# Optimization experiments

Measured on AMD Instinct MI355X. Metric: run time of the kernel, lower is better.

The kernel has to match this reference:

```python
import jax, jax.numpy as jnp
import numpy as np

B_, L_, D_MODEL = 2, 2048, 2048
EXPAND = 2
D_IN = EXPAND * D_MODEL            # 4096 intermediate_size
HEADS = 64
HEAD_DIM = D_IN // HEADS           # 64
STATE = 128
NGROUPS = 1
K = 4                              # conv kernel
CONV_DIM = D_IN + 2 * NGROUPS * STATE   # 4352
PROJ = D_IN + CONV_DIM + HEADS          # 8512
CHUNK = 256
EPS = 1e-5


def setup_inputs() -> dict:
    key = jax.random.key(0)
    ks = jax.random.split(key, 4)
    return {
        "hidden_states": jax.random.normal(ks[0], (B_, L_, D_MODEL), jnp.float32),
        "in_proj_w": jax.random.normal(ks[1], (PROJ, D_MODEL), jnp.float32) * 0.02,
        "conv_w": jax.random.normal(ks[2], (CONV_DIM, K), jnp.float32) * 0.2,
        "conv_b": jnp.zeros((CONV_DIM,), jnp.float32),
        "dt_bias": jnp.ones((HEADS,), jnp.float32),
        "A_log": jnp.log(jnp.arange(1, HEADS + 1, dtype=jnp.float32)),
        "D": jnp.ones((HEADS,), jnp.float32),
        "norm_w": jnp.ones((D_IN,), jnp.float32),
        "out_proj_w": jax.random.normal(ks[3], (D_MODEL, D_IN), jnp.float32) * 0.02,
    }


def _segsum(x):
    # x: [..., T] -> lower-triangular segment sums [..., T, T]
    T = x.shape[-1]
    c = jnp.cumsum(x, axis=-1)
    seg = c[..., :, None] - c[..., None, :]
    return jnp.where(jnp.tril(jnp.ones((T, T), bool)), seg, -jnp.inf)


def _ssd(x, dA, Bm, Cm):
    # chunked SSD scan (exact math of the sequential selective scan)
    # x: [b,l,h,p] (already * dt), dA: [b,l,h], Bm/Cm: [b,l,g,n]
    b, l, h, p = x.shape
    n = Bm.shape[-1]
    c = l // CHUNK
    rep = h // Bm.shape[2]
    Bh = jnp.repeat(Bm, rep, axis=2).reshape(b, c, CHUNK, h, n)
    Ch = jnp.repeat(Cm, rep, axis=2).reshape(b, c, CHUNK, h, n)
    x = x.reshape(b, c, CHUNK, h, p)
    dA = dA.reshape(b, c, CHUNK, h).transpose(0, 3, 1, 2)       # [b,h,c,cl]
    dA_cum = jnp.cumsum(dA, axis=-1)
    Lmat = jnp.exp(_segsum(dA))                                  # [b,h,c,cl,cl]
    # intra-chunk (diagonal) contribution
    Y_diag = jnp.einsum('bcthn,bcshn,bhcts,bcshp->bcthp', Ch, Bh, Lmat, x)
    # per-chunk final states
    decay_states = jnp.exp(dA_cum[..., -1:] - dA_cum)            # [b,h,c,cl]
    states = jnp.einsum('bcshn,bhcs,bcshp->bchpn', Bh, decay_states, x)
    # inter-chunk recurrence
    chunk_decay = jnp.exp(_segsum(jnp.pad(dA_cum[..., -1], ((0, 0), (0, 0), (1, 0)))))  # [b,h,c+1,c+1]
    states = jnp.concatenate([jnp.zeros_like(states[:, :1]), states], axis=1)
    prev = jnp.einsum('bhzc,bchpn->bzhpn', chunk_decay, states)[:, :-1]  # state entering each chunk
    Y_off = jnp.einsum('bcthn,bchpn,bhct->bcthp', Ch, prev, jnp.exp(dA_cum))
    return (Y_diag + Y_off).reshape(b, l, h, p)


def reference(hidden_states, in_proj_w, conv_w, conv_b, dt_bias, A_log, D, norm_w, out_proj_w):
    b, l, _ = hidden_states.shape
    proj = hidden_states @ in_proj_w.T                     # [b,l,PROJ]
    gate = proj[..., :D_IN]
    xBC = proj[..., D_IN:D_IN + CONV_DIM]
    dt = proj[..., D_IN + CONV_DIM:]                       # [b,l,H]
    # causal depthwise conv1d (padding=K-1, truncated to seq_len) + silu
    xp = jnp.pad(xBC, ((0, 0), (K - 1, 0), (0, 0)))
    conv = conv_b + sum(conv_w[:, i] * xp[:, i:i + l, :] for i in range(K))
    xBC = jax.nn.silu(conv)
    x = xBC[..., :D_IN].reshape(b, l, HEADS, HEAD_DIM)
    Bm = xBC[..., D_IN:D_IN + NGROUPS * STATE].reshape(b, l, NGROUPS, STATE)
    Cm = xBC[..., D_IN + NGROUPS * STATE:].reshape(b, l, NGROUPS, STATE)
    dt = jax.nn.softplus(dt + dt_bias)                     # time_step_limit=(0,inf): no clamp
    A = -jnp.exp(A_log)                                    # [H]
    y = _ssd(x * dt[..., None], dt * A, Bm, Cm)            # [b,l,H,P]
    y = y + D[None, None, :, None] * x                     # skip term D*x
    y = y.reshape(b, l, D_IN)
    # MambaRMSNormGated: gate then rms-normalize
    hg = y * jax.nn.silu(gate)
    var = jnp.mean(hg * hg, axis=-1, keepdims=True)
    y = hg * jax.lax.rsqrt(var + EPS) * norm_w
    return y @ out_proj_w.T
```

## Files before the change

kernel.cpp:

```cpp
#include <hip/hip_runtime.h>
#include <hip/hip_bf16.h>
#include <cstdio>

#define LQ 2048
#define BB 2
#define BL 4096
#define DMODEL 2048
#define DIN 4096
#define NH 64
#define HD 64
#define NST 128
#define CONVD 4352
#define PROJD 8512
#define PROJ_PAD2 8704
#define PXW 4416
#define CHK 256
#define NCH 8

typedef __attribute__((ext_vector_type(8))) short short8;
typedef __attribute__((ext_vector_type(4))) float f32x4;

__device__ __forceinline__ unsigned short f2bu(float x) {
  __hip_bfloat16 h = __float2bfloat16(x);
  return __builtin_bit_cast(unsigned short, h);
}

__device__ __forceinline__ float b2f(unsigned short u) {
  return __bfloat162float(__builtin_bit_cast(__hip_bfloat16, u));
}

__device__ __forceinline__ f32x4 mfma16(short8 a, short8 b, f32x4 c) {
  return __builtin_amdgcn_mfma_f32_16x16x32_bf16(a, b, c, 0, 0, 0);
}

#define GLD16(gptr, lptr)                                                  \
  __builtin_amdgcn_global_load_lds(                                        \
      (const __attribute__((address_space(1))) void*)(gptr),               \
      (__attribute__((address_space(3))) void*)(lptr), 16, 0, 0)

__global__ void k_cast3(const float* __restrict__ s0, unsigned short* __restrict__ d0,
                        long n0,
                        const float* __restrict__ s1, unsigned short* __restrict__ d1,
                        long n1r, long n1t,
                        const float* __restrict__ s2, unsigned short* __restrict__ d2,
                        long n2) {
  const long ntot8 = (n0 + n1t + n2) >> 3;
  long i = (long)blockIdx.x * blockDim.x + threadIdx.x;
  const long stride = (long)gridDim.x * blockDim.x;
  for (; i < ntot8; i += stride) {
    const long e = i << 3;
    const float* src;
    unsigned short* dst;
    long rel, nreal;
    if (e < n0) { src = s0; dst = d0; rel = e; nreal = n0; }
    else if (e < n0 + n1t) { src = s1; dst = d1; rel = e - n0; nreal = n1r; }
    else { src = s2; dst = d2; rel = e - n0 - n1t; nreal = n2; }
    short8 pk;
    if (rel + 8 <= nreal) {
      const f32x4* sp = reinterpret_cast<const f32x4*>(src + rel);
      f32x4 v0 = sp[0], v1 = sp[1];
#pragma unroll
      for (int u = 0; u < 4; u++) {
        pk[u] = (short)f2bu(v0[u]);
        pk[4 + u] = (short)f2bu(v1[u]);
      }
    } else {
#pragma unroll
      for (int u = 0; u < 8; u++)
        pk[u] = (rel + u < nreal) ? (short)f2bu(src[rel + u]) : (short)0;
    }
    *reinterpret_cast<short8*>(dst + rel) = pk;
  }
}

__device__ __forceinline__ short8 rdfrag(const unsigned short (*mp)[64], int rowbase,
                                         int lane, int kh) {
  const int row = rowbase + (lane & 15);
  const int cg = (((kh << 2) + (lane >> 4)) ^ (lane & 7)) << 3;
  return *reinterpret_cast<const short8*>(&mp[row][cg]);
}

template <bool SPLIT>
__global__ __launch_bounds__(512) void k_gemm256(
    const unsigned short* __restrict__ A, const unsigned short* __restrict__ Bw,
    float* __restrict__ C, unsigned short* __restrict__ gateb,
    float* __restrict__ projx, int Nreal, int K) {
  __shared__ unsigned short sh[2][2][256][64];
  const int tid = threadIdx.x;
  const int lane = tid & 63, w = tid >> 6;
  const int wm = w >> 2, wn2 = w & 3;
  const int gx = gridDim.x;
  const int nwg = gx * gridDim.y;
  const int bid = blockIdx.y * gx + blockIdx.x;
  const int qq = nwg >> 3;
  const int swz = (bid & 7) * qq + (bid >> 3);
  const int m0 = (swz / gx) * 256, n0 = (swz % gx) * 256;
  const int srow = tid >> 3;
  const int sdst = (tid & 7) * 8;
  const int ssrc = ((tid & 7) ^ ((tid >> 3) & 7)) * 8;
  const unsigned short* Ab = A + (size_t)m0 * K;
  const unsigned short* Bb = Bw + (size_t)n0 * K;

#define ST(bf, mt, MP, r0, kk)                                             \
  GLD16(MP + (size_t)((r0) + srow) * K + (kk) + ssrc,                      \
        &sh[bf][mt][(r0) + srow][sdst])

  f32x4 acc[8][4] = {};
  const int nt = K >> 6;

  ST(0, 0, Ab, 0, 0);   ST(0, 0, Ab, 128, 0);
  ST(0, 1, Bb, 0, 0);   ST(0, 1, Bb, 64, 0);
  ST(0, 1, Bb, 128, 0); ST(0, 1, Bb, 192, 0);
  ST(0, 0, Ab, 64, 0);  ST(0, 0, Ab, 192, 0);

#define DO_PHASE(P)                                                        \
  {                                                                        \
    const int rb = wm * 128 + (P) * 32;                                    \
    short8 a00 = rdfrag(sh[cur][0], rb, lane, 0);                          \
    short8 a01 = rdfrag(sh[cur][0], rb, lane, 1);                          \
    short8 a10 = rdfrag(sh[cur][0], rb + 16, lane, 0);                     \
    short8 a11 = rdfrag(sh[cur][0], rb + 16, lane, 1);                     \
    __builtin_amdgcn_s_setprio(1);                                         \
    _Pragma("unroll")                                                      \
    for (int nf = 0; nf < 4; nf++) {                                       \
      acc[2 * (P)][nf] = mfma16(a00, bfr[nf][0], acc[2 * (P)][nf]);        \
      acc[2 * (P)][nf] = mfma16(a01, bfr[nf][1], acc[2 * (P)][nf]);        \
      acc[2 * (P) + 1][nf] = mfma16(a10, bfr[nf][0], acc[2 * (P) + 1][nf]);\
      acc[2 * (P) + 1][nf] = mfma16(a11, bfr[nf][1], acc[2 * (P) + 1][nf]);\
    }                                                                      \
    __builtin_amdgcn_s_setprio(0);                                         \
  }

  for (int t = 0; t < nt; ++t) {
    const int cur = t & 1, nxt = cur ^ 1;
    const int kbn = (t + 1) << 6;
    const bool more = (t + 1 < nt);
    asm volatile("s_waitcnt vmcnt(2)" ::: "memory");
    __builtin_amdgcn_s_barrier();
    if (more) { ST(nxt, 0, Ab, 0, kbn); ST(nxt, 0, Ab, 128, kbn); }
    short8 bfr[4][2];
#pragma unroll
    for (int nf = 0; nf < 4; nf++) {
      bfr[nf][0] = rdfrag(sh[cur][1], wn2 * 64 + nf * 16, lane, 0);
      bfr[nf][1] = rdfrag(sh[cur][1], wn2 * 64 + nf * 16, lane, 1);
    }
    DO_PHASE(0)
    __builtin_amdgcn_s_barrier();
    if (more) { ST(nxt, 1, Bb, 0, kbn); ST(nxt, 1, Bb, 64, kbn); }
    DO_PHASE(1)
    if (more) asm volatile("s_waitcnt vmcnt(4)" ::: "memory");
    else      asm volatile("s_waitcnt vmcnt(0)" ::: "memory");
    __builtin_amdgcn_s_barrier();
    if (more) { ST(nxt, 1, Bb, 128, kbn); ST(nxt, 1, Bb, 192, kbn); }
    DO_PHASE(2)
    __builtin_amdgcn_s_barrier();
    if (more) { ST(nxt, 0, Ab, 64, kbn); ST(nxt, 0, Ab, 192, kbn); }
    DO_PHASE(3)
  }
#undef DO_PHASE
#undef ST

#pragma unroll
  for (int mf = 0; mf < 8; mf++) {
    const int row = m0 + wm * 128 + mf * 16 + ((lane >> 4) << 2);
#pragma unroll
    for (int nf = 0; nf < 4; nf++) {
      const int col = n0 + wn2 * 64 + nf * 16 + (lane & 15);
      if (SPLIT) {
        if (col < DIN) {
#pragma unroll
          for (int v = 0; v < 4; v++)
            gateb[(size_t)(row + v) * DIN + col] = f2bu(acc[mf][nf][v]);
        } else if (col < PROJD) {
#pragma unroll
          for (int v = 0; v < 4; v++)
            projx[(size_t)(row + v) * PXW + (col - DIN)] = acc[mf][nf][v];
        }
      } else {
        if (col < Nreal) {
#pragma unroll
          for (int v = 0; v < 4; v++)
            C[(size_t)(row + v) * Nreal + col] = acc[mf][nf][v];
        }
      }
    }
  }
}

__global__ __launch_bounds__(256) void k_gemm_bt(
    const unsigned short* __restrict__ A, const unsigned short* __restrict__ Bw,
    float* __restrict__ C, int Nreal, int K) {
  __shared__ unsigned short lA[128][64];
  __shared__ unsigned short lB[128][64];
  const int tid = threadIdx.x;
  const int lane = tid & 63, w = tid >> 6;
  const int gx = gridDim.x;
  const int nwg = gx * gridDim.y;
  const int bid = blockIdx.y * gx + blockIdx.x;
  const int qq = nwg >> 3;
  const int swz = (bid & 7) * qq + (bid >> 3);
  const int m0 = (swz / gx) * 128, n0 = (swz % gx) * 128;
  const int wr = (w >> 1) * 64, wc = (w & 1) * 64;
  const int sr = tid >> 3;
  const int sdst = (tid & 7) * 8;
  const int ssrc = ((tid & 7) ^ ((tid >> 3) & 7)) * 8;
  f32x4 acc[4][4] = {};
  for (int kb = 0; kb < K; kb += 64) {
#pragma unroll
    for (int i = 0; i < 4; i++) {
      const int r = sr + i * 32;
      GLD16(A + (size_t)(m0 + r) * K + kb + ssrc, &lA[r][sdst]);
      GLD16(Bw + (size_t)(n0 + r) * K + kb + ssrc, &lB[r][sdst]);
    }
    __syncthreads();
#pragma unroll
    for (int kk = 0; kk < 64; kk += 32) {
      short8 af[4], bf[4];
      const int cg = ((((kk >> 3) + (lane >> 4)) ^ (lane & 7)) << 3);
#pragma unroll
      for (int i = 0; i < 4; i++) {
        af[i] = *reinterpret_cast<const short8*>(&lA[wr + i * 16 + (lane & 15)][cg]);
        bf[i] = *reinterpret_cast<const short8*>(&lB[wc + i * 16 + (lane & 15)][cg]);
      }
#pragma unroll
      for (int mi = 0; mi < 4; mi++)
#pragma unroll
        for (int ni = 0; ni < 4; ni++)
          acc[mi][ni] = mfma16(af[mi], bf[ni], acc[mi][ni]);
    }
    __syncthreads();
  }
#pragma unroll
  for (int mi = 0; mi < 4; mi++) {
    const int row = m0 + wr + mi * 16 + ((lane >> 4) << 2);
#pragma unroll
    for (int ni = 0; ni < 4; ni++) {
      const int col = n0 + wc + ni * 16 + (lane & 15);
      if (col < Nreal) {
#pragma unroll
        for (int v = 0; v < 4; v++)
          C[(size_t)(row + v) * Nreal + col] = acc[mi][ni][v];
      }
    }
  }
}

__global__ __launch_bounds__(256) void k_conv_silu(
    const float* __restrict__ projx, const float* __restrict__ cw,
    const float* __restrict__ cb, unsigned short* __restrict__ xbc) {
  const int ch = blockIdx.x * 256 + threadIdx.x;
  const int bt = blockIdx.y;
  const int b = bt >> 11, t = bt & 2047;
  float acc = cb[ch];
#pragma unroll
  for (int i = 0; i < 4; i++) {
    int tt = t - 3 + i;
    if (tt >= 0)
      acc += cw[ch * 4 + i] * projx[((size_t)b * LQ + tt) * PXW + ch];
  }
  float o = acc / (1.f + __expf(-acc));
  xbc[(size_t)bt * CONVD + ch] = f2bu(o);
}

__global__ __launch_bounds__(256) void k_dt(
    const float* __restrict__ projx, const float* __restrict__ dtb,
    const float* __restrict__ alog, float* __restrict__ dtv,
    float* __restrict__ dac) {
  const int bc = blockIdx.x;
  const int b = bc >> 3, c = bc & 7;
  const int h = threadIdx.x & 63, q = threadIdx.x >> 6;
  const float bias = dtb[h];
  const float Ah = -__expf(alog[h]);
  const size_t base = (size_t)b * LQ + c * CHK + q * 64;
  float vals[64];
  float part = 0.f;
#pragma unroll
  for (int j = 0; j < 64; j++) {
    float raw = projx[(base + j) * PXW + CONVD + h] + bias;
    float dt = raw > 20.f ? raw : log1pf(__expf(raw));
    vals[j] = dt;
    dtv[(base + j) * NH + h] = dt;
    part += dt;
  }
  __shared__ float partials[4][64];
  partials[q][h] = part;
  __syncthreads();
  float cum = 0.f;
  for (int qq = 0; qq < q; qq++) cum += partials[qq][h];
  cum *= Ah;
#pragma unroll
  for (int j = 0; j < 64; j++) {
    cum += vals[j] * Ah;
    dac[(base + j) * NH + h] = cum;
  }
}

__global__ __launch_bounds__(256) void k_cb(const unsigned short* __restrict__ xbc,
                                            float* __restrict__ cbuf) {
  const int q = blockIdx.x;
  const int bc = blockIdx.y;
  const int b = bc >> 3, c = bc & 7;
  const int qt = q >> 1, qs = q & 1;
  __shared__ unsigned short lC[128][136];
  __shared__ unsigned short lB[128][136];
  const int tid = threadIdx.x, lane = tid & 63, w = tid >> 6;
  {
    int r = tid >> 1, hf = tid & 1;
    size_t rowc = (size_t)b * LQ + c * CHK + qt * 128 + r;
    size_t rowb = (size_t)b * LQ + c * CHK + qs * 128 + r;
    const unsigned short* crp = xbc + rowc * CONVD + DIN + NST + hf * 64;
    const unsigned short* brp = xbc + rowb * CONVD + DIN + hf * 64;
#pragma unroll
    for (int n8 = 0; n8 < 8; n8++) {
      *reinterpret_cast<short8*>(&lC[r][hf * 64 + n8 * 8]) =
          *reinterpret_cast<const short8*>(crp + n8 * 8);
      *reinterpret_cast<short8*>(&lB[r][hf * 64 + n8 * 8]) =
          *reinterpret_cast<const short8*>(brp + n8 * 8);
    }
  }
  __syncthreads();
  const int wr = (w >> 1) * 64, wc = (w & 1) * 64;
  f32x4 acc[4][4] = {};
#pragma unroll
  for (int kk = 0; kk < 128; kk += 32) {
    short8 a[4], bb[4];
    const int ko = kk + ((lane >> 4) << 3);
#pragma unroll
    for (int i = 0; i < 4; i++) {
      a[i] = *reinterpret_cast<const short8*>(&lC[wr + i * 16 + (lane & 15)][ko]);
      bb[i] = *reinterpret_cast<const short8*>(&lB[wc + i * 16 + (lane & 15)][ko]);
    }
#pragma unroll
    for (int mi = 0; mi < 4; mi++)
#pragma unroll
      for (int ni = 0; ni < 4; ni++)
        acc[mi][ni] = mfma16(a[mi], bb[ni], acc[mi][ni]);
  }
  float* outp = cbuf + (size_t)bc * (CHK * CHK);
#pragma unroll
  for (int mi = 0; mi < 4; mi++) {
    const int t = qt * 128 + wr + mi * 16 + ((lane >> 4) << 2);
#pragma unroll
    for (int ni = 0; ni < 4; ni++) {
      const int s = qs * 128 + wc + ni * 16 + (lane & 15);
#pragma unroll
      for (int v = 0; v < 4; v++)
        outp[(size_t)(t + v) * CHK + s] = acc[mi][ni][v];
    }
  }
}

__global__ __launch_bounds__(256) void k_diag(
    const unsigned short* __restrict__ xbc, const float* __restrict__ dtv,
    const float* __restrict__ dac, const float* __restrict__ cbuf,
    float* __restrict__ y, float* __restrict__ st) {
  const int h = blockIdx.x, c = blockIdx.y, b = blockIdx.z;
  const int cs = c * CHK;
  __shared__ unsigned short lXt[64][136];
  __shared__ unsigned short lBt[128][136];
  __shared__ unsigned short lS[256][40];
  __shared__ float lda[256];
  __shared__ float lesE[256];
  const int tid = threadIdx.x, lane = tid & 63, w = tid >> 6;
  lda[tid] = dac[((size_t)b * LQ + cs + tid) * NH + h];
  __syncthreads();
  lesE[tid] = __expf(lda[tid | 31] - lda[tid]);
  const float dalast = lda[255];
  const float* cbp = cbuf + ((size_t)(b * NCH + c)) * (CHK * CHK);
  const float da_t = lda[tid];
  f32x4 accY[4][4] = {};
  f32x4 accS[4][2] = {};
  const int wn = w * 32;
  const int sl = tid & 127, sub = tid >> 7;
  for (int half = 0; half < 2; half++) {
    {
      const int s = half * 128 + sl;
      const size_t row = (size_t)b * LQ + cs + s;
      const unsigned short* xrow = xbc + row * CONVD;
      const float dts = dtv[row * NH + h];
      const float dec = __expf(dalast - lda[s]);
#pragma unroll
      for (int g = 0; g < 4; g++) {
        short8 xv = *reinterpret_cast<const short8*>(xrow + h * HD + sub * 32 + g * 8);
#pragma unroll
        for (int u = 0; u < 8; u++)
          lXt[sub * 32 + g * 8 + u][sl] = f2bu(b2f((unsigned short)xv[u]) * dts);
      }
#pragma unroll
      for (int g = 0; g < 8; g++) {
        short8 bv = *reinterpret_cast<const short8*>(xrow + DIN + sub * 64 + g * 8);
#pragma unroll
        for (int u = 0; u < 8; u++)
          lBt[sub * 64 + g * 8 + u][sl] = f2bu(b2f((unsigned short)bv[u]) * dec);
      }
    }
    __syncthreads();
    for (int sb4 = 0; sb4 < 4; sb4++) {
      const int sb = half * 4 + sb4;
      {
        const int t = tid;
        const int tb = t >> 5;
        if (tb > sb) {
          const float et = __expf(da_t - lda[sb * 32 + 31]);
          const f32x4* cr = reinterpret_cast<const f32x4*>(cbp + (size_t)t * CHK + sb * 32);
          f32x4 vv[8];
#pragma unroll
          for (int j4 = 0; j4 < 8; j4++) vv[j4] = cr[j4];
#pragma unroll
          for (int g = 0; g < 4; g++) {
            short8 pk;
#pragma unroll
            for (int e = 0; e < 8; e++) {
              const int j = g * 8 + e;
              pk[e] = (short)f2bu(vv[j >> 2][j & 3] * et * lesE[sb * 32 + j]);
            }
            *reinterpret_cast<short8*>(&lS[t][g * 8]) = pk;
          }
        } else if (tb == sb) {
          const f32x4* cr = reinterpret_cast<const f32x4*>(cbp + (size_t)t * CHK + sb * 32);
          f32x4 vv[8];
#pragma unroll
          for (int j4 = 0; j4 < 8; j4++) vv[j4] = cr[j4];
          const int tl = t & 31;
#pragma unroll
          for (int g = 0; g < 4; g++) {
            short8 pk;
#pragma unroll
            for (int e = 0; e < 8; e++) {
              const int j = g * 8 + e;
              float val = (j <= tl)
                  ? vv[j >> 2][j & 3] * __expf(da_t - lda[sb * 32 + j]) : 0.f;
              pk[e] = (short)f2bu(val);
            }
            *reinterpret_cast<short8*>(&lS[t][g * 8]) = pk;
          }
        } else {
          short8 z = {};
#pragma unroll
          for (int g = 0; g < 4; g++)
            *reinterpret_cast<short8*>(&lS[tid][g * 8]) = z;
        }
      }
      __syncthreads();
      short8 sf[4], xf[4], btf[2];
      const int ko = ((lane >> 4) << 3);
      const int so = sb4 * 32 + ko;
#pragma unroll
      for (int i = 0; i < 4; i++) {
        sf[i] = *reinterpret_cast<const short8*>(&lS[w * 64 + i * 16 + (lane & 15)][ko]);
        xf[i] = *reinterpret_cast<const short8*>(&lXt[i * 16 + (lane & 15)][so]);
      }
#pragma unroll
      for (int i = 0; i < 2; i++)
        btf[i] = *reinterpret_cast<const short8*>(&lBt[wn + i * 16 + (lane & 15)][so]);
#pragma unroll
      for (int mi = 0; mi < 4; mi++)
#pragma unroll
        for (int ni = 0; ni < 4; ni++)
          accY[mi][ni] = mfma16(sf[mi], xf[ni], accY[mi][ni]);
#pragma unroll
      for (int mi = 0; mi < 4; mi++)
#pragma unroll
        for (int nj = 0; nj < 2; nj++)
          accS[mi][nj] = mfma16(xf[mi], btf[nj], accS[mi][nj]);
      __syncthreads();
    }
  }
#pragma unroll
  for (int mi = 0; mi < 4; mi++) {
    const int t = w * 64 + mi * 16 + ((lane >> 4) << 2);
#pragma unroll
    for (int ni = 0; ni < 4; ni++) {
      const int p = ni * 16 + (lane & 15);
#pragma unroll
      for (int v = 0; v < 4; v++)
        y[((size_t)b * LQ + cs + t + v) * DIN + h * HD + p] = accY[mi][ni][v];
    }
  }
  float* stp = st + ((size_t)((b * NCH + c) * NH + h)) * (HD * NST);
#pragma unroll
  for (int mi = 0; mi < 4; mi++) {
    const int p = mi * 16 + ((lane >> 4) << 2);
#pragma unroll
    for (int nj = 0; nj < 2; nj++) {
      const int n = wn + nj * 16 + (lane & 15);
#pragma unroll
      for (int v = 0; v < 4; v++)
        stp[(size_t)(p + v) * NST + n] = accS[mi][nj][v];
    }
  }
}

__global__ void k_scan(const float* __restrict__ st, const float* __restrict__ dac,
                       unsigned short* __restrict__ pv) {
  const int h = blockIdx.x, b = blockIdx.y;
  const int tid = threadIdx.x;
  float P[32];
#pragma unroll
  for (int j = 0; j < 32; j++) P[j] = 0.f;
  for (int c = 0; c < NCH; c++) {
    const size_t base = ((size_t)((b * NCH + c) * NH + h)) * (HD * NST);
#pragma unroll
    for (int j = 0; j < 32; j++) pv[base + tid + 256 * j] = f2bu(P[j]);
    const float d = __expf(dac[((size_t)b * LQ + c * CHK + 255) * NH + h]);
#pragma unroll
    for (int j = 0; j < 32; j++) P[j] = P[j] * d + st[base + tid + 256 * j];
  }
}

__global__ __launch_bounds__(256) void k_off(
    const unsigned short* __restrict__ xbc, const float* __restrict__ dac,
    const unsigned short* __restrict__ pv, const float* __restrict__ Dp,
    float* __restrict__ y) {
  const int h = blockIdx.x;
  const int cth = blockIdx.y;
  const int c = cth >> 1, th = cth & 1;
  const int b = blockIdx.z;
  const int cs = c * CHK, t0 = th * 128;
  __shared__ unsigned short lC[128][136];
  __shared__ unsigned short lP[64][136];
  __shared__ float lda[128];
  const int tid = threadIdx.x, lane = tid & 63, w = tid >> 6;
  const int wt = w >> 1, wp = w & 1;
  {
    const int r = tid >> 1, hf = tid & 1;
    const size_t row = (size_t)b * LQ + cs + t0 + r;
    if (hf == 0) lda[r] = dac[row * NH + h];
    const unsigned short* cr = xbc + row * CONVD + DIN + NST + hf * 64;
#pragma unroll
    for (int n8 = 0; n8 < 8; n8++)
      *reinterpret_cast<short8*>(&lC[r][hf * 64 + n8 * 8]) =
          *reinterpret_cast<const short8*>(cr + n8 * 8);
  }
  if (tid < 64) {
    const unsigned short* pr =
        pv + ((size_t)((b * NCH + c) * NH + h)) * (HD * NST) + (size_t)tid * NST;
#pragma unroll
    for (int n8 = 0; n8 < 16; n8++)
      *reinterpret_cast<short8*>(&lP[tid][n8 * 8]) =
          *reinterpret_cast<const short8*>(pr + n8 * 8);
  }
  __syncthreads();
  f32x4 acc[4][2] = {};
#pragma unroll
  for (int kk = 0; kk < 128; kk += 32) {
    short8 a[4], bb[2];
    const int ko = kk + ((lane >> 4) << 3);
#pragma unroll
    for (int i = 0; i < 4; i++)
      a[i] = *reinterpret_cast<const short8*>(&lC[wt * 64 + i * 16 + (lane & 15)][ko]);
#pragma unroll
    for (int j = 0; j < 2; j++)
      bb[j] = *reinterpret_cast<const short8*>(&lP[wp * 32 + j * 16 + (lane & 15)][ko]);
#pragma unroll
    for (int mi = 0; mi < 4; mi++)
#pragma unroll
      for (int nj = 0; nj < 2; nj++)
        acc[mi][nj] = mfma16(a[mi], bb[nj], acc[mi][nj]);
  }
  const float Dh = Dp[h];
#pragma unroll
  for (int mi = 0; mi < 4; mi++) {
    const int tl = wt * 64 + mi * 16 + ((lane >> 4) << 2);
#pragma unroll
    for (int nj = 0; nj < 2; nj++) {
      const int p = wp * 32 + nj * 16 + (lane & 15);
#pragma unroll
      for (int v = 0; v < 4; v++) {
        const int tt = tl + v;
        const size_t row = (size_t)b * LQ + cs + t0 + tt;
        const float scale = __expf(lda[tt]);
        const float xval = b2f(xbc[row * CONVD + h * HD + p]);
        const size_t yi = row * DIN + h * HD + p;
        y[yi] += scale * acc[mi][nj][v] + Dh * xval;
      }
    }
  }
}

__global__ __launch_bounds__(256) void k_gatenorm(
    const float* __restrict__ y, const unsigned short* __restrict__ gateb,
    const float* __restrict__ nw, unsigned short* __restrict__ hgb) {
  const int r = blockIdx.x;
  const int tid = threadIdx.x;
  const float* yr = y + (size_t)r * DIN;
  const unsigned short* gr = gateb + (size_t)r * DIN;
  float hg[16];
  float ss = 0.f;
#pragma unroll
  for (int j = 0; j < 16; j++) {
    const int d = tid + 256 * j;
    const float g = b2f(gr[d]);
    const float v = yr[d] * (g / (1.f + __expf(-g)));
    hg[j] = v;
    ss += v * v;
  }
#pragma unroll
  for (int o = 32; o > 0; o >>= 1) ss += __shfl_down(ss, o);
  __shared__ float red[4];
  if ((tid & 63) == 0) red[tid >> 6] = ss;
  __syncthreads();
  const float tot = red[0] + red[1] + red[2] + red[3];
  const float scale = rsqrtf(tot / (float)DIN + 1e-5f);
#pragma unroll
  for (int j = 0; j < 16; j++) {
    const int d = tid + 256 * j;
    hgb[(size_t)r * DIN + d] = f2bu(hg[j] * scale * nw[d]);
  }
}

extern "C" void kernel_launch(void* const* d_in, const int* in_sizes, int n_in,
                              void* d_out, int out_size, void* d_ws, size_t ws_size,
                              hipStream_t stream) {
  const float* hidden = (const float*)d_in[0];
  const float* w1 = (const float*)d_in[1];
  const float* cw = (const float*)d_in[2];
  const float* cb = (const float*)d_in[3];
  const float* dtb = (const float*)d_in[4];
  const float* alog = (const float*)d_in[5];
  const float* Dp = (const float*)d_in[6];
  const float* nw = (const float*)d_in[7];
  const float* w2 = (const float*)d_in[8];
  float* out = (float*)d_out;
  char* ws = (char*)d_ws;

  const size_t OFF_GATEB = 0;
  const size_t OFF_XBC = 33554432;
  const size_t OFF_DTV = 104857600;
  const size_t OFF_DAC = 105906176;
  const size_t OFF_CB = 106954752;
  const size_t OFF_Y = 111149056;
  const size_t OFF_ST = 178257920;
  const size_t OFF_PV = 211812352;
  const size_t OFF_PROJX = 111149056;
  const size_t OFF_HB = 183500800;
  const size_t OFF_W1B = 200278016;
  const size_t OFF_W2B = 245366784;
  const size_t OFF_HGB = 33554432;
  const size_t NEED = 262144000;
  if (ws_size < NEED) {
    fprintf(stderr, "WS TOO SMALL: %zu < %zu\n", ws_size, NEED);
    return;
  }
  unsigned short* gateb = (unsigned short*)(ws + OFF_GATEB);
  unsigned short* xbc = (unsigned short*)(ws + OFF_XBC);
  float* dtv = (float*)(ws + OFF_DTV);
  float* dac = (float*)(ws + OFF_DAC);
  float* cbuf = (float*)(ws + OFF_CB);
  float* y = (float*)(ws + OFF_Y);
  float* st = (float*)(ws + OFF_ST);
  unsigned short* pv = (unsigned short*)(ws + OFF_PV);
  float* projx = (float*)(ws + OFF_PROJX);
  unsigned short* hb = (unsigned short*)(ws + OFF_HB);
  unsigned short* w1b = (unsigned short*)(ws + OFF_W1B);
  unsigned short* w2b = (unsigned short*)(ws + OFF_W2B);
  unsigned short* hgb = (unsigned short*)(ws + OFF_HGB);

  k_cast3<<<4096, 256, 0, stream>>>(hidden, hb, (long)BL * DMODEL,
                                    w1, w1b, (long)PROJD * DMODEL,
                                    (long)PROJ_PAD2 * DMODEL,
                                    w2, w2b, (long)DMODEL * DIN);
  k_gemm256<true><<<dim3(PROJ_PAD2 / 256, BL / 256), 512, 0, stream>>>(
      hb, w1b, nullptr, gateb, projx, PROJD, DMODEL);
  k_conv_silu<<<dim3(17, BL), 256, 0, stream>>>(projx, cw, cb, xbc);
  k_dt<<<16, 256, 0, stream>>>(projx, dtb, alog, dtv, dac);
  k_cb<<<dim3(4, 16), 256, 0, stream>>>(xbc, cbuf);
  k_diag<<<dim3(NH, NCH, BB), 256, 0, stream>>>(xbc, dtv, dac, cbuf, y, st);
  k_scan<<<dim3(NH, BB), 256, 0, stream>>>(st, dac, pv);
  k_off<<<dim3(NH, NCH * 2, BB), 256, 0, stream>>>(xbc, dac, pv, Dp, y);
  k_gatenorm<<<BL, 256, 0, stream>>>(y, gateb, nw, hgb);
  k_gemm_bt<<<dim3(DMODEL / 128, BL / 128), 256, 0, stream>>>(
      hgb, w2b, out, DMODEL, DIN);
}
```

Before: 551.4 us.

## Split states from diag, fuse off-diagonal into Y kernel, vectorize gatenorm

Moves the chunk-state computation out of the diagonal kernel into a dedicated k_states kernel that writes bf16 states. The intra-chunk and inter-chunk contributions plus the D skip term are now computed in a single k_y kernel. This removes the read-modify-write of y in the old off-diagonal pass and one fp32 write/read of y. The gatenorm kernel switches to contiguous vectorized loads and stores per thread. The trade-offs are extra redundant loads of x across the two kernels and lower precision from storing states in bf16.

```diff
diff --git a/kernel.cpp b/kernel.cpp
--- a/kernel.cpp
+++ b/kernel.cpp
@@ -350,14 +350,101 @@
   }
 }
 
-__global__ __launch_bounds__(256) void k_diag(
+__global__ __launch_bounds__(256) void k_states(
     const unsigned short* __restrict__ xbc, const float* __restrict__ dtv,
-    const float* __restrict__ dac, const float* __restrict__ cbuf,
-    float* __restrict__ y, float* __restrict__ st) {
+    const float* __restrict__ dac, unsigned short* __restrict__ st) {
   const int h = blockIdx.x, c = blockIdx.y, b = blockIdx.z;
   const int cs = c * CHK;
   __shared__ unsigned short lXt[64][136];
   __shared__ unsigned short lBt[128][136];
+  __shared__ float lda[256];
+  const int tid = threadIdx.x, lane = tid & 63, w = tid >> 6;
+  lda[tid] = dac[((size_t)b * LQ + cs + tid) * NH + h];
+  __syncthreads();
+  const float dalast = lda[255];
+  f32x4 accS[4][2] = {};
+  const int wn = w * 32;
+  const int sl = tid & 127, sub = tid >> 7;
+  for (int half = 0; half < 2; half++) {
+    if (half) __syncthreads();
+    {
+      const int s = half * 128 + sl;
+      const size_t row = (size_t)b * LQ + cs + s;
+      const unsigned short* xrow = xbc + row * CONVD;
+      const float dts = dtv[row * NH + h];
+      const float dec = __expf(dalast - lda[s]);
+#pragma unroll
+      for (int g = 0; g < 4; g++) {
+        short8 xv = *reinterpret_cast<const short8*>(xrow + h * HD + sub * 32 + g * 8);
+#pragma unroll
+        for (int u = 0; u < 8; u++)
+          lXt[sub * 32 + g * 8 + u][sl] = f2bu(b2f((unsigned short)xv[u]) * dts);
+      }
+#pragma unroll
+      for (int g = 0; g < 8; g++) {
+        short8 bv = *reinterpret_cast<const short8*>(xrow + DIN + sub * 64 + g * 8);
+#pragma unroll
+        for (int u = 0; u < 8; u++)
+          lBt[sub * 64 + g * 8 + u][sl] = f2bu(b2f((unsigned short)bv[u]) * dec);
+      }
+    }
+    __syncthreads();
+    for (int sb4 = 0; sb4 < 4; sb4++) {
+      short8 xf[4], btf[2];
+      const int so = sb4 * 32 + ((lane >> 4) << 3);
+#pragma unroll
+      for (int i = 0; i < 4; i++)
+        xf[i] = *reinterpret_cast<const short8*>(&lXt[i * 16 + (lane & 15)][so]);
+#pragma unroll
+      for (int i = 0; i < 2; i++)
+        btf[i] = *reinterpret_cast<const short8*>(&lBt[wn + i * 16 + (lane & 15)][so]);
+#pragma unroll
+      for (int mi = 0; mi < 4; mi++)
+#pragma unroll
+        for (int nj = 0; nj < 2; nj++)
+          accS[mi][nj] = mfma16(xf[mi], btf[nj], accS[mi][nj]);
+    }
+  }
+  unsigned short* stp = st + ((size_t)((b * NCH + c) * NH + h)) * (HD * NST);
+#pragma unroll
+  for (int mi = 0; mi < 4; mi++) {
+    const int p = mi * 16 + ((lane >> 4) << 2);
+#pragma unroll
+    for (int nj = 0; nj < 2; nj++) {
+      const int n = wn + nj * 16 + (lane & 15);
+#pragma unroll
+      for (int v = 0; v < 4; v++)
+        stp[(size_t)(p + v) * NST + n] = f2bu(accS[mi][nj][v]);
+    }
+  }
+}
+
+__global__ void k_scan(const unsigned short* __restrict__ st,
+                       const float* __restrict__ dac,
+                       unsigned short* __restrict__ pv) {
+  const int h = blockIdx.x, b = blockIdx.y;
+  const int tid = threadIdx.x;
+  float P[32];
+#pragma unroll
+  for (int j = 0; j < 32; j++) P[j] = 0.f;
+  for (int c = 0; c < NCH; c++) {
+    const size_t base = ((size_t)((b * NCH + c) * NH + h)) * (HD * NST);
+#pragma unroll
+    for (int j = 0; j < 32; j++) pv[base + tid + 256 * j] = f2bu(P[j]);
+    const float d = __expf(dac[((size_t)b * LQ + c * CHK + 255) * NH + h]);
+#pragma unroll
+    for (int j = 0; j < 32; j++) P[j] = P[j] * d + b2f(st[base + tid + 256 * j]);
+  }
+}
+
+__global__ __launch_bounds__(256) void k_y(
+    const unsigned short* __restrict__ xbc, const float* __restrict__ dtv,
+    const float* __restrict__ dac, const float* __restrict__ cbuf,
+    const unsigned short* __restrict__ pv, const float* __restrict__ Dp,
+    float* __restrict__ y) {
+  const int h = blockIdx.x, c = blockIdx.y, b = blockIdx.z;
+  const int cs = c * CHK;
+  __shared__ unsigned short lXt[64][136];
   __shared__ unsigned short lS[256][40];
   __shared__ float lda[256];
   __shared__ float lesE[256];
@@ -365,12 +452,9 @@
   lda[tid] = dac[((size_t)b * LQ + cs + tid) * NH + h];
   __syncthreads();
   lesE[tid] = __expf(lda[tid | 31] - lda[tid]);
-  const float dalast = lda[255];
+  const float da_t = lda[tid];
   const float* cbp = cbuf + ((size_t)(b * NCH + c)) * (CHK * CHK);
-  const float da_t = lda[tid];
   f32x4 accY[4][4] = {};
-  f32x4 accS[4][2] = {};
-  const int wn = w * 32;
   const int sl = tid & 127, sub = tid >> 7;
   for (int half = 0; half < 2; half++) {
     {
@@ -378,20 +462,12 @@
       const size_t row = (size_t)b * LQ + cs + s;
       const unsigned short* xrow = xbc + row * CONVD;
       const float dts = dtv[row * NH + h];
-      const float dec = __expf(dalast - lda[s]);
 #pragma unroll
       for (int g = 0; g < 4; g++) {
         short8 xv = *reinterpret_cast<const short8*>(xrow + h * HD + sub * 32 + g * 8);
 #pragma unroll
         for (int u = 0; u < 8; u++)
           lXt[sub * 32 + g * 8 + u][sl] = f2bu(b2f((unsigned short)xv[u]) * dts);
-      }
-#pragma unroll
-      for (int g = 0; g < 8; g++) {
-        short8 bv = *reinterpret_cast<const short8*>(xrow + DIN + sub * 64 + g * 8);
-#pragma unroll
-        for (int u = 0; u < 8; u++)
-          lBt[sub * 64 + g * 8 + u][sl] = f2bu(b2f((unsigned short)bv[u]) * dec);
       }
     }
     __syncthreads();
@@ -442,7 +518,7 @@
         }
       }
       __syncthreads();
-      short8 sf[4], xf[4], btf[2];
+      short8 sf[4], xf[4];
       const int ko = ((lane >> 4) << 3);
       const int so = sb4 * 32 + ko;
 #pragma unroll
@@ -451,21 +527,55 @@
         xf[i] = *reinterpret_cast<const short8*>(&lXt[i * 16 + (lane & 15)][so]);
       }
 #pragma unroll
-      for (int i = 0; i < 2; i++)
-        btf[i] = *reinterpret_cast<const short8*>(&lBt[wn + i * 16 + (lane & 15)][so]);
-#pragma unroll
       for (int mi = 0; mi < 4; mi++)
 #pragma unroll
         for (int ni = 0; ni < 4; ni++)
           accY[mi][ni] = mfma16(sf[mi], xf[ni], accY[mi][ni]);
-#pragma unroll
-      for (int mi = 0; mi < 4; mi++)
-#pragma unroll
-        for (int nj = 0; nj < 2; nj++)
-          accS[mi][nj] = mfma16(xf[mi], btf[nj], accS[mi][nj]);
       __syncthreads();
     }
   }
+  {
+    const unsigned short* pr =
+        pv + ((size_t)((b * NCH + c) * NH + h)) * (HD * NST);
+    const int p = tid >> 2, qtr = tid & 3;
+#pragma unroll
+    for (int g = 0; g < 4; g++)
+      *reinterpret_cast<short8*>(&lXt[p][qtr * 32 + g * 8]) =
+          *reinterpret_cast<const short8*>(pr + (size_t)p * NST + qtr * 32 + g * 8);
+  }
+  __syncthreads();
+  const float et_self = __expf(da_t);
+  const unsigned short* crow =
+      xbc + ((size_t)b * LQ + cs + tid) * CONVD + DIN + NST;
+  for (int sb4 = 0; sb4 < 4; sb4++) {
+    {
+#pragma unroll
+      for (int g = 0; g < 4; g++) {
+        short8 cv = *reinterpret_cast<const short8*>(crow + sb4 * 32 + g * 8);
+        short8 pk;
+#pragma unroll
+        for (int e = 0; e < 8; e++)
+          pk[e] = (short)f2bu(b2f((unsigned short)cv[e]) * et_self);
+        *reinterpret_cast<short8*>(&lS[tid][g * 8]) = pk;
+      }
+    }
+    __syncthreads();
+    short8 sf[4], xf[4];
+    const int ko = ((lane >> 4) << 3);
+    const int so = sb4 * 32 + ko;
+#pragma unroll
+    for (int i = 0; i < 4; i++) {
+      sf[i] = *reinterpret_cast<const short8*>(&lS[w * 64 + i * 16 + (lane & 15)][ko]);
+      xf[i] = *reinterpret_cast<const short8*>(&lXt[i * 16 + (lane & 15)][so]);
+    }
+#pragma unroll
+    for (int mi = 0; mi < 4; mi++)
+#pragma unroll
+      for (int ni = 0; ni < 4; ni++)
+        accY[mi][ni] = mfma16(sf[mi], xf[ni], accY[mi][ni]);
+    __syncthreads();
+  }
+  const float Dh = Dp[h];
 #pragma unroll
   for (int mi = 0; mi < 4; mi++) {
     const int t = w * 64 + mi * 16 + ((lane >> 4) << 2);
@@ -473,106 +583,10 @@
     for (int ni = 0; ni < 4; ni++) {
       const int p = ni * 16 + (lane & 15);
 #pragma unroll
-      for (int v = 0; v < 4; v++)
-        y[((size_t)b * LQ + cs + t + v) * DIN + h * HD + p] = accY[mi][ni][v];
-    }
-  }
-  float* stp = st + ((size_t)((b * NCH + c) * NH + h)) * (HD * NST);
-#pragma unroll
-  for (int mi = 0; mi < 4; mi++) {
-    const int p = mi * 16 + ((lane >> 4) << 2);
-#pragma unroll
-    for (int nj = 0; nj < 2; nj++) {
-      const int n = wn + nj * 16 + (lane & 15);
-#pragma unroll
-      for (int v = 0; v < 4; v++)
-        stp[(size_t)(p + v) * NST + n] = accS[mi][nj][v];
-    }
-  }
-}
-
-__global__ void k_scan(const float* __restrict__ st, const float* __restrict__ dac,
-                       unsigned short* __restrict__ pv) {
-  const int h = blockIdx.x, b = blockIdx.y;
-  const int tid = threadIdx.x;
-  float P[32];
-#pragma unroll
-  for (int j = 0; j < 32; j++) P[j] = 0.f;
-  for (int c = 0; c < NCH; c++) {
-    const size_t base = ((size_t)((b * NCH + c) * NH + h)) * (HD * NST);
-#pragma unroll
-    for (int j = 0; j < 32; j++) pv[base + tid + 256 * j] = f2bu(P[j]);
-    const float d = __expf(dac[((size_t)b * LQ + c * CHK + 255) * NH + h]);
-#pragma unroll
-    for (int j = 0; j < 32; j++) P[j] = P[j] * d + st[base + tid + 256 * j];
-  }
-}
-
-__global__ __launch_bounds__(256) void k_off(
-    const unsigned short* __restrict__ xbc, const float* __restrict__ dac,
-    const unsigned short* __restrict__ pv, const float* __restrict__ Dp,
-    float* __restrict__ y) {
-  const int h = blockIdx.x;
-  const int cth = blockIdx.y;
-  const int c = cth >> 1, th = cth & 1;
-  const int b = blockIdx.z;
-  const int cs = c * CHK, t0 = th * 128;
-  __shared__ unsigned short lC[128][136];
-  __shared__ unsigned short lP[64][136];
-  __shared__ float lda[128];
-  const int tid = threadIdx.x, lane = tid & 63, w = tid >> 6;
-  const int wt = w >> 1, wp = w & 1;
-  {
-    const int r = tid >> 1, hf = tid & 1;
-    const size_t row = (size_t)b * LQ + cs + t0 + r;
-    if (hf == 0) lda[r] = dac[row * NH + h];
-    const unsigned short* cr = xbc + row * CONVD + DIN + NST + hf * 64;
-#pragma unroll
-    for (int n8 = 0; n8 < 8; n8++)
-      *reinterpret_cast<short8*>(&lC[r][hf * 64 + n8 * 8]) =
-          *reinterpret_cast<const short8*>(cr + n8 * 8);
-  }
-  if (tid < 64) {
-    const unsigned short* pr =
-        pv + ((size_t)((b * NCH + c) * NH + h)) * (HD * NST) + (size_t)tid * NST;
-#pragma unroll
-    for (int n8 = 0; n8 < 16; n8++)
-      *reinterpret_cast<short8*>(&lP[tid][n8 * 8]) =
-          *reinterpret_cast<const short8*>(pr + n8 * 8);
-  }
-  __syncthreads();
-  f32x4 acc[4][2] = {};
-#pragma unroll
-  for (int kk = 0; kk < 128; kk += 32) {
-    short8 a[4], bb[2];
-    const int ko = kk + ((lane >> 4) << 3);
-#pragma unroll
-    for (int i = 0; i < 4; i++)
-      a[i] = *reinterpret_cast<const short8*>(&lC[wt * 64 + i * 16 + (lane & 15)][ko]);
-#pragma unroll
-    for (int j = 0; j < 2; j++)
-      bb[j] = *reinterpret_cast<const short8*>(&lP[wp * 32 + j * 16 + (lane & 15)][ko]);
-#pragma unroll
-    for (int mi = 0; mi < 4; mi++)
-#pragma unroll
-      for (int nj = 0; nj < 2; nj++)
-        acc[mi][nj] = mfma16(a[mi], bb[nj], acc[mi][nj]);
-  }
-  const float Dh = Dp[h];
-#pragma unroll
-  for (int mi = 0; mi < 4; mi++) {
-    const int tl = wt * 64 + mi * 16 + ((lane >> 4) << 2);
-#pragma unroll
-    for (int nj = 0; nj < 2; nj++) {
-      const int p = wp * 32 + nj * 16 + (lane & 15);
-#pragma unroll
       for (int v = 0; v < 4; v++) {
-        const int tt = tl + v;
-        const size_t row = (size_t)b * LQ + cs + t0 + tt;
-        const float scale = __expf(lda[tt]);
+        const size_t row = (size_t)b * LQ + cs + t + v;
         const float xval = b2f(xbc[row * CONVD + h * HD + p]);
-        const size_t yi = row * DIN + h * HD + p;
-        y[yi] += scale * acc[mi][nj][v] + Dh * xval;
+        y[row * DIN + h * HD + p] = accY[mi][ni][v] + Dh * xval;
       }
     }
   }
@@ -583,15 +597,21 @@
     const float* __restrict__ nw, unsigned short* __restrict__ hgb) {
   const int r = blockIdx.x;
   const int tid = threadIdx.x;
-  const float* yr = y + (size_t)r * DIN;
-  const unsigned short* gr = gateb + (size_t)r * DIN;
+  const int d0 = tid * 16;
+  const float* yr = y + (size_t)r * DIN + d0;
+  const unsigned short* gr = gateb + (size_t)r * DIN + d0;
+  f32x4 yv[4];
+  short8 gv[2];
+#pragma unroll
+  for (int q = 0; q < 4; q++) yv[q] = reinterpret_cast<const f32x4*>(yr)[q];
+#pragma unroll
+  for (int q = 0; q < 2; q++) gv[q] = reinterpret_cast<const short8*>(gr)[q];
   float hg[16];
   float ss = 0.f;
 #pragma unroll
   for (int j = 0; j < 16; j++) {
-    const int d = tid + 256 * j;
-    const float g = b2f(gr[d]);
-    const float v = yr[d] * (g / (1.f + __expf(-g)));
+    const float g = b2f((unsigned short)gv[j >> 3][j & 7]);
+    const float v = yv[j >> 2][j & 3] * (g / (1.f + __expf(-g)));
     hg[j] = v;
     ss += v * v;
   }
@@ -602,11 +622,17 @@
   __syncthreads();
   const float tot = red[0] + red[1] + red[2] + red[3];
   const float scale = rsqrtf(tot / (float)DIN + 1e-5f);
+  const float* nr = nw + d0;
+  short8 o0, o1;
 #pragma unroll
   for (int j = 0; j < 16; j++) {
-    const int d = tid + 256 * j;
-    hgb[(size_t)r * DIN + d] = f2bu(hg[j] * scale * nw[d]);
-  }
+    const unsigned short ov = f2bu(hg[j] * scale * nr[j]);
+    if (j < 8) o0[j] = (short)ov;
+    else o1[j - 8] = (short)ov;
+  }
+  unsigned short* hp = hgb + (size_t)r * DIN + d0;
+  *reinterpret_cast<short8*>(hp) = o0;
+  *reinterpret_cast<short8*>(hp + 8) = o1;
 }
 
 extern "C" void kernel_launch(void* const* d_in, const int* in_sizes, int n_in,
@@ -648,7 +674,7 @@
   float* dac = (float*)(ws + OFF_DAC);
   float* cbuf = (float*)(ws + OFF_CB);
   float* y = (float*)(ws + OFF_Y);
-  float* st = (float*)(ws + OFF_ST);
+  unsigned short* st = (unsigned short*)(ws + OFF_ST);
   unsigned short* pv = (unsigned short*)(ws + OFF_PV);
   float* projx = (float*)(ws + OFF_PROJX);
   unsigned short* hb = (unsigned short*)(ws + OFF_HB);
@@ -665,9 +691,9 @@
   k_conv_silu<<<dim3(17, BL), 256, 0, stream>>>(projx, cw, cb, xbc);
   k_dt<<<16, 256, 0, stream>>>(projx, dtb, alog, dtv, dac);
   k_cb<<<dim3(4, 16), 256, 0, stream>>>(xbc, cbuf);
-  k_diag<<<dim3(NH, NCH, BB), 256, 0, stream>>>(xbc, dtv, dac, cbuf, y, st);
+  k_states<<<dim3(NH, NCH, BB), 256, 0, stream>>>(xbc, dtv, dac, st);
   k_scan<<<dim3(NH, BB), 256, 0, stream>>>(st, dac, pv);
-  k_off<<<dim3(NH, NCH * 2, BB), 256, 0, stream>>>(xbc, dac, pv, Dp, y);
+  k_y<<<dim3(NH, NCH, BB), 256, 0, stream>>>(xbc, dtv, dac, cbuf, pv, Dp, y);
   k_gatenorm<<<BL, 256, 0, stream>>>(y, gateb, nw, hgb);
   k_gemm_bt<<<dim3(DMODEL / 128, BL / 128), 256, 0, stream>>>(
       hgb, w2b, out, DMODEL, DIN);
```

New measurement: 550.1 us. No clear change (-0.2%).
